# Performance work log

Measured on AMD Instinct MI355X. Metric: run time of the kernel, lower is better.

## Reference

```python
import jax, jax.numpy as jnp
import numpy as np

B, U, I, H = 4096, 6, 1024, 512
IK, IV, K = 64, 400, 4
CH, CK, CV = 4, 32, 512
NS = 4


def setup_inputs() -> dict:
    key = jax.random.key(0)
    ks = jax.random.split(key, 14)
    s = 0.02
    return dict(
        x=jax.random.normal(ks[0], (B, 1, I), jnp.float32),
        hs=jax.random.normal(ks[1], (B, U, H), jnp.float32),
        Wk=jax.random.normal(ks[2], (I, IK), jnp.float32) * s,
        bk=jnp.zeros((IK,), jnp.float32),
        Wv=jax.random.normal(ks[3], (I, IV), jnp.float32) * s,
        bv=jnp.zeros((IV,), jnp.float32),
        Wq=jax.random.normal(ks[4], (U, H, IK), jnp.float32) * s,
        Wq_=jax.random.normal(ks[5], (U, H, CH * CK), jnp.float32) * s,
        Wk_=jax.random.normal(ks[6], (U, H, CH * CK), jnp.float32) * s,
        Wv_=jax.random.normal(ks[7], (U, H, CH * CV), jnp.float32) * s,
        Wo_=jax.random.normal(ks[8], (U, CH * CV, CV), jnp.float32) * s,
        sw=jax.nn.softmax(jax.random.normal(ks[9], (U, NS), jnp.float32), axis=-1),
        gru_wx=jax.random.normal(ks[10], (NS, IV, 3 * H), jnp.float32) * s,
        gru_wh=jax.random.normal(ks[11], (NS, H, 3 * H), jnp.float32) * s,
    )


def reference(x, hs, Wk, bk, Wv, bv, Wq, Wq_, Wk_, Wv_, Wo_, sw, gru_wx, gru_wh):
    b = x.shape[0]
    # append null input along token dim -> (B, 2, I)
    x2 = jnp.concatenate([x, jnp.zeros_like(x)], axis=1)
    # input attention (num_input_heads = 1)
    k_l = x2 @ Wk + bk                                   # (B,2,IK)
    v_l = x2 @ Wv + bv                                   # (B,2,IV)
    q_l = jnp.einsum('buh,uhd->bud', hs, Wq)             # (B,U,IK)
    scores = jnp.einsum('bud,btd->but', q_l, k_l) / np.sqrt(IK).astype(np.float32)
    # top-k gating on the non-null score
    not_null = scores[:, :, 0]                           # (B,U)
    _, idx = jax.lax.top_k(not_null, K)
    mask = jnp.zeros((b, U), x.dtype).at[jnp.arange(b)[:, None], idx].set(1.0)
    probs = jax.nn.softmax(scores, axis=-1)              # dropout off (eval)
    inputs = jnp.einsum('but,btv->buv', probs, v_l) * mask[:, :, None]  # (B,U,IV)
    # shared-schema GroupGRU: per-unit weights = schema mixture
    Wx = jnp.einsum('us,sio->uio', sw, gru_wx)           # (U,IV,3H)
    Wh = jnp.einsum('us,sho->uho', sw, gru_wh)           # (U,H,3H)
    gx = jnp.einsum('bui,uio->buo', inputs, Wx)
    gh = jnp.einsum('buh,uho->buo', hs, Wh)
    xr, xz, xn = jnp.split(gx, 3, axis=-1)
    hr, hz, hn = jnp.split(gh, 3, axis=-1)
    r = jax.nn.sigmoid(xr + hr)
    z = jax.nn.sigmoid(xz + hz)
    n = jnp.tanh(xn + r * hn)
    hy = n + z * (hs - n)                                # (B,U,H)
    # blocked_grad is identity in forward
    h_b = hy
    # communication attention (4 heads)
    q = jnp.einsum('buh,uho->buo', h_b, Wq_).reshape(b, U, CH, CK).transpose(0, 2, 1, 3)
    kk = jnp.einsum('buh,uho->buo', h_b, Wk_).reshape(b, U, CH, CK).transpose(0, 2, 1, 3)
    v = jnp.einsum('buh,uho->buo', h_b, Wv_).reshape(b, U, CH, CV).transpose(0, 2, 1, 3)
    att = jnp.einsum('bhqd,bhkd->bhqk', q, kk) / np.sqrt(CK).astype(np.float32)
    ap = jax.nn.softmax(att, axis=-1) * mask[:, None, :, None]  # mask query units
    ctx = jnp.einsum('bhqk,bhkd->bhqd', ap, v)           # (B,CH,U,CV)
    ctx = ctx.transpose(0, 2, 1, 3).reshape(b, U, CH * CV)
    ctx = jnp.einsum('buh,uho->buo', ctx, Wo_) + h_b     # (B,U,H)
    m = mask[:, :, None]
    hs_new = m * ctx + (1.0 - m) * hs
    return hs_new
```

## Files before the change

### kernel.cpp

```cpp
#include <hip/hip_runtime.h>
#include <cstddef>
#include <cstdint>


typedef unsigned short u16;
typedef __bf16 bf16x8 __attribute__((ext_vector_type(8)));
typedef float f32x4 __attribute__((ext_vector_type(4)));
typedef u16 u16x4 __attribute__((ext_vector_type(4)));

#define DEVFN static __device__ __forceinline__

DEVFN float ldin(const void* p, size_t i, int f) {
  return f ? (float)reinterpret_cast<const __bf16*>(p)[i]
           : reinterpret_cast<const float*>(p)[i];
}
DEVFN float bf2f(const u16* p, size_t i) {
  return (float)reinterpret_cast<const __bf16*>(p)[i];
}
DEVFN void f2bf(u16* p, size_t i, float v) {
  reinterpret_cast<__bf16*>(p)[i] = (__bf16)v;
}
DEVFN u16 bfbits(float v) {
  __bf16 b = (__bf16)v;
  return *reinterpret_cast<u16*>(&b);
}
DEVFN void gload16(const __bf16* g, __bf16* l) {
  __builtin_amdgcn_global_load_lds(
      (const __attribute__((address_space(1))) void*)g,
      (__attribute__((address_space(3))) void*)l, 16, 0, 0);
}

constexpr size_t OFF_FLAG = 0;
constexpr size_t OFF_MASK = 256;
constexpr size_t OFF_WVT  = 98560;
constexpr size_t OFF_WQKV = 1147136;
constexpr size_t OFF_WOT  = 15302912;
constexpr size_t OFF_WXCT = 27885824;
constexpr size_t OFF_WHCT = 35553536;
constexpr size_t OFF_HY   = 44990720;
constexpr size_t OFF_XB   = 70156544;
constexpr size_t OFF_HSB  = 78545152;
constexpr size_t ARENA    = 103710976;
constexpr size_t A_INP    = ARENA;
constexpr size_t A_PK     = ARENA;
constexpr size_t A_PQ     = ARENA + 4194304;
constexpr size_t A_P1     = 124158208;
constexpr size_t A_KL     = A_P1;
constexpr size_t A_QL     = A_P1 + 1048576;
constexpr size_t A_VL     = A_P1 + 7340032;

__global__ void rim_detect(const void* sw, int* flagp) {
  if (threadIdx.x == 0) {
    float s = 0.f;
    for (int i = 0; i < 24; i++)
      s += (float)reinterpret_cast<const __bf16*>(sw)[i];
    flagp[0] = (s > 5.5f && s < 6.5f) ? 1 : 0;
  }
}

__global__ __launch_bounds__(256)
void rim_cast(const void* __restrict__ in, u16* __restrict__ out, long n8,
              const int* __restrict__ flagp)
{
  const int f = flagp[0];
  long stride = (long)gridDim.x * 256;
  for (long u = (long)blockIdx.x * 256 + threadIdx.x; u < n8; u += stride) {
    if (f) {
      reinterpret_cast<uint4*>(out)[u] = reinterpret_cast<const uint4*>(in)[u];
    } else {
      f32x4 lo = reinterpret_cast<const f32x4*>(in)[u * 2];
      f32x4 hi = reinterpret_cast<const f32x4*>(in)[u * 2 + 1];
      bf16x8 r;
#pragma unroll
      for (int q = 0; q < 4; q++) { r[q] = (__bf16)lo[q]; r[q + 4] = (__bf16)hi[q]; }
      reinterpret_cast<bf16x8*>(out)[u] = r;
    }
  }
}

__global__ __launch_bounds__(256)
void rim_sgemm32(const void* __restrict__ A_, long lda, long Az,
                 const void* __restrict__ W_, long Wz,
                 float* __restrict__ P, int KC,
                 const int* __restrict__ flagp)
{
  const int f = flagp[0];
  __shared__ float As[32 * 33];
  __shared__ float Ws[32 * 68];
  const int t = threadIdx.x;
  const int m0 = blockIdx.x * 32, kc = blockIdx.y, z = blockIdx.z;
  const int Z = gridDim.z;
  const int kb = kc * KC;
  const int tx = t & 15, ty = t >> 4;

  f32x4 acc[2];
#pragma unroll
  for (int i = 0; i < 2; i++)
#pragma unroll
    for (int j = 0; j < 4; j++) acc[i][j] = 0.f;

  for (int k0 = kb; k0 < kb + KC; k0 += 32) {
#pragma unroll
    for (int j = 0; j < 4; j++) {
      int idx = t + j * 256;
      int row = idx >> 5, kk = idx & 31;
      As[row * 33 + kk] =
          ldin(A_, (size_t)(m0 + row) * lda + (size_t)z * Az + k0 + kk, f);
    }
#pragma unroll
    for (int j = 0; j < 8; j++) {
      int idx = t + j * 256;
      int kk = idx >> 6, n = idx & 63;
      Ws[kk * 68 + n] = ldin(W_, (size_t)z * Wz + (size_t)(k0 + kk) * 64 + n, f);
    }
    __syncthreads();
#pragma unroll 8
    for (int kk = 0; kk < 32; kk++) {
      f32x4 wv = *reinterpret_cast<const f32x4*>(&Ws[kk * 68 + tx * 4]);
#pragma unroll
      for (int i = 0; i < 2; i++) {
        float a = As[(ty * 2 + i) * 33 + kk];
#pragma unroll
        for (int j = 0; j < 4; j++) acc[i][j] += a * wv[j];
      }
    }
    __syncthreads();
  }
  float* Pb = P + ((size_t)kc * Z + z) * (4096 * 64);
#pragma unroll
  for (int i = 0; i < 2; i++)
    *reinterpret_cast<f32x4*>(&Pb[(size_t)(m0 + ty * 2 + i) * 64 + tx * 4]) = acc[i];
}

__global__ void rim_sreduce(const float* __restrict__ P, int NK, int Z,
                            float* __restrict__ C, long ldc, long Cz,
                            const void* __restrict__ bias,
                            const int* __restrict__ flagp, long total)
{
  const int f = flagp[0];
  long idx = (long)blockIdx.x * 256 + threadIdx.x;
  if (idx >= total) return;
  long z = idx / (4096 * 64);
  long r = idx - z * (4096 * 64);
  long m = r >> 6;
  int n = (int)(r & 63);
  float s = bias ? ldin(bias, n, f) : 0.f;
  for (int kc = 0; kc < NK; kc++)
    s += P[((size_t)kc * Z + z) * (4096 * 64) + r];
  C[(size_t)m * ldc + (size_t)z * Cz + n] = s;
}

template<int EPI>
__global__ __launch_bounds__(256)
void rim_gemm(const u16* __restrict__ A16, long A0, long lda, long Az,
              const u16* __restrict__ B_, long Bz,
              void* __restrict__ C_, long C0, long ldc, long Cz,
              int M, int N, int K,
              const void* __restrict__ bias,
              const u16* __restrict__ hyp,
              const float* __restrict__ maskp,
              const void* __restrict__ hsp,
              const int* __restrict__ flagp)
{
  __shared__ __align__(16) __bf16 As[2][128 * 32];
  __shared__ __align__(16) __bf16 Bs[2][128 * 32];
  const int f = flagp[0];
  const int t = threadIdx.x;

  int gx = gridDim.x, gy = gridDim.y;
  int nwg = gx * gy * (int)gridDim.z;
  int wg = blockIdx.x + gx * (blockIdx.y + gy * blockIdx.z);
  {
    int q = nwg >> 3, r = nwg & 7, xc = wg & 7, ix = wg >> 3;
    wg = (xc < r ? xc * (q + 1) : r * (q + 1) + (xc - r) * q) + ix;
  }
  const int mb = wg % gx;
  const int nb = (wg / gx) % gy;
  const int z  = wg / (gx * gy);
  const int m0 = mb * 128, n0 = nb * 128;

  const __bf16* Ab = reinterpret_cast<const __bf16*>(A16) + (size_t)A0 +
                     (size_t)z * Az + (size_t)m0 * lda;
  const __bf16* Bb = reinterpret_cast<const __bf16*>(B_) + (size_t)z * Bz +
                     (size_t)n0 * (size_t)K;

  const int lane = t & 63, w = t >> 6;
  const int srow = lane >> 2;
  const int skq  = (lane & 3) * 8;
  const __bf16* aS0 = Ab + (size_t)(w * 16 + srow) * lda + skq;
  const __bf16* aS1 = Ab + (size_t)((w + 4) * 16 + srow) * lda + skq;
  const __bf16* bS0 = Bb + (size_t)(w * 16 + srow) * (size_t)K + skq;
  const __bf16* bS1 = Bb + (size_t)((w + 4) * 16 + srow) * (size_t)K + skq;

  const int wm = (w & 1) * 64, wn = (w >> 1) * 64;
  const int lr = lane & 15, lk = (lane >> 4) * 8;

  f32x4 acc[4][4];
#pragma unroll
  for (int i = 0; i < 4; i++)
#pragma unroll
    for (int j = 0; j < 4; j++)
#pragma unroll
      for (int r = 0; r < 4; r++) acc[i][j][r] = 0.f;

  auto STAGE = [&](int buf, int k0) {
    gload16(aS0 + k0, &As[buf][w * 512]);
    gload16(aS1 + k0, &As[buf][(w + 4) * 512]);
    gload16(bS0 + k0, &Bs[buf][w * 512]);
    gload16(bS1 + k0, &Bs[buf][(w + 4) * 512]);
  };

  STAGE(0, 0);
  int cur = 0;
  for (int k0 = 0; k0 < K; k0 += 32) {
    __syncthreads();
    if (k0 + 32 < K) STAGE(cur ^ 1, k0 + 32);
    bf16x8 af[4], bg[4];
#pragma unroll
    for (int i = 0; i < 4; i++)
      af[i] = *reinterpret_cast<const bf16x8*>(&As[cur][(wm + i * 16 + lr) * 32 + lk]);
#pragma unroll
    for (int j = 0; j < 4; j++)
      bg[j] = *reinterpret_cast<const bf16x8*>(&Bs[cur][(wn + j * 16 + lr) * 32 + lk]);
#pragma unroll
    for (int i = 0; i < 4; i++)
#pragma unroll
      for (int j = 0; j < 4; j++)
        acc[i][j] = __builtin_amdgcn_mfma_f32_16x16x32_bf16(af[i], bg[j], acc[i][j], 0, 0, 0);
    cur ^= 1;
  }

  const int rq = (lane >> 4) * 4;
  const int cq = lane & 15;
#pragma unroll
  for (int i = 0; i < 4; i++) {
#pragma unroll
    for (int j = 0; j < 4; j++) {
      int cg = n0 + wn + j * 16 + cq;
      if (cg >= N) continue;
#pragma unroll
      for (int r = 0; r < 4; r++) {
        int rg = m0 + wm + i * 16 + rq + r;
        if (rg >= M) continue;
        float v = acc[i][j][r];
        size_t cidx = (size_t)rg * ldc + (size_t)z * Cz + cg;
        if constexpr (EPI == 2) {
          f2bf((u16*)C_, C0 + cidx, v + ldin(bias, cg, f));
        } else if constexpr (EPI == 3) {
          f2bf((u16*)C_, C0 + cidx, v);
        } else {
          float mk = maskp[(size_t)rg * 6 + z];
          if (mk > 0.5f) {
            float o = v + bf2f(hyp, cidx);
            if (f) f2bf((u16*)C_, C0 + cidx, o);
            else   reinterpret_cast<float*>(C_)[C0 + cidx] = o;
          } else {
            if (f) reinterpret_cast<u16*>(C_)[C0 + cidx] =
                       reinterpret_cast<const u16*>(hsp)[C0 + cidx];
            else   reinterpret_cast<float*>(C_)[C0 + cidx] =
                       reinterpret_cast<const float*>(hsp)[C0 + cidx];
          }
        }
      }
    }
  }
}

__global__ __launch_bounds__(256)
void rim_transpose(const void* __restrict__ in, u16* __restrict__ out,
                   int N, int Np, int K, long in_z, long out_z,
                   const int* __restrict__ flagp)
{
  const int f = flagp[0];
  __shared__ float tile[32][33];
  int z = blockIdx.z;
  int k0 = blockIdx.x * 32, n0 = blockIdx.y * 32;
  int c = threadIdx.x & 31, r = threadIdx.x >> 5;
  for (int rr = r; rr < 32; rr += 8) {
    int k = k0 + rr, n = n0 + c;
    tile[rr][c] = (k < K && n < N)
        ? ldin(in, (size_t)z * in_z + (size_t)k * N + n, f) : 0.f;
  }
  __syncthreads();
  for (int rr = r; rr < 32; rr += 8) {
    int n = n0 + rr, k = k0 + c;
    if (n < Np && k < K)
      f2bf(out, (size_t)z * out_z + (size_t)n * K + k, tile[c][rr]);
  }
}

__global__ __launch_bounds__(256)
void rim_gruw(const void* __restrict__ sw, const void* __restrict__ gw,
              u16* __restrict__ out, int IVp, int IVs,
              const int* __restrict__ flagp)
{
  const int f = flagp[0];
  __shared__ float lds[64 * 17];
  int u = blockIdx.z;
  int i0 = blockIdx.x * 16, o0 = blockIdx.y * 64;
  int t = threadIdx.x;
  float s0 = ldin(sw, u * 4 + 0, f), s1 = ldin(sw, u * 4 + 1, f);
  float s2 = ldin(sw, u * 4 + 2, f), s3 = ldin(sw, u * 4 + 3, f);
  int oo = t & 63, iq = t >> 6;
  size_t pl = (size_t)IVs * 1536;
#pragma unroll
  for (int r = 0; r < 4; r++) {
    int ii = iq * 4 + r;
    float acc = 0.f;
    if (i0 + ii < IVs) {
      size_t base = (size_t)(i0 + ii) * 1536 + o0 + oo;
      acc = s0 * ldin(gw, base, f) + s1 * ldin(gw, pl + base, f) +
            s2 * ldin(gw, 2 * pl + base, f) + s3 * ldin(gw, 3 * pl + base, f);
    }
    lds[oo * 17 + ii] = acc;
  }
  __syncthreads();
  int ow = t >> 2, iw = (t & 3) * 4;
  u16x4 pk;
#pragma unroll
  for (int j = 0; j < 4; j++) pk[j] = bfbits(lds[ow * 17 + iw + j]);
  *reinterpret_cast<u16x4*>(out + ((size_t)u * 1536 + o0 + ow) * IVp + i0 + iw) = pk;
}

__global__ __launch_bounds__(256)
void rim_scores(const float* __restrict__ q_l, const float* __restrict__ k_l0,
                const void* __restrict__ bk, const u16* __restrict__ v_l0,
                const void* __restrict__ bv, float* __restrict__ maskf,
                u16* __restrict__ inputs, const int* __restrict__ flagp)
{
  const int f = flagp[0];
  int b = blockIdx.x;
  int t = threadIdx.x;
  int lane = t & 63;
  __shared__ float s0[6], s1[6], sm[6], sp[6];
  if (t < 64) {
    float kv = k_l0[(size_t)b * 64 + lane];
    for (int u = 0; u < 6; u++) {
      float p = q_l[((size_t)b * 6 + u) * 64 + lane] * kv;
      for (int off = 32; off; off >>= 1) p += __shfl_down(p, off);
      if (lane == 0) s0[u] = p * 0.125f;
    }
  } else if (t < 128) {
    float kv = ldin(bk, lane, f);
    for (int u = 0; u < 6; u++) {
      float p = q_l[((size_t)b * 6 + u) * 64 + lane] * kv;
      for (int off = 32; off; off >>= 1) p += __shfl_down(p, off);
      if (lane == 0) s1[u] = p * 0.125f;
    }
  }
  __syncthreads();
  if (t == 0) {
    for (int u = 0; u < 6; u++) {
      int cnt = 0;
      for (int u2 = 0; u2 < 6; u2++)
        if (s0[u2] > s0[u] || (s0[u2] == s0[u] && u2 < u)) cnt++;
      float mk = (cnt < 4) ? 1.0f : 0.0f;
      sm[u] = mk;
      maskf[(size_t)b * 6 + u] = mk;
      sp[u] = 1.0f / (1.0f + expf(s1[u] - s0[u]));
    }
  }
  __syncthreads();
  for (int idx = t; idx < 2496; idx += 256) {
    int u = idx / 416, j = idx - u * 416;
    float val = 0.f;
    if (j < 400)
      val = sm[u] * (sp[u] * bf2f(v_l0, (size_t)b * 400 + j) +
                     (1.0f - sp[u]) * ldin(bv, j, f));
    f2bf(inputs, ((size_t)b * 6 + u) * 416 + j, val);
  }
}

__global__ void rim_gru(const u16* __restrict__ Ggx, const u16* __restrict__ Ggh,
                        const void* __restrict__ hs, long R0,
                        u16* __restrict__ hy, long total,
                        const int* __restrict__ flagp)
{
  const int f = flagp[0];
  long idx = (long)blockIdx.x * 256 + threadIdx.x;
  if (idx >= total) return;
  long bu = idx >> 9;
  int h = idx & 511;
  size_t gb = (size_t)bu * 1536 + h;
  float xr = bf2f(Ggx, gb), xz = bf2f(Ggx, gb + 512), xn = bf2f(Ggx, gb + 1024);
  float hr = bf2f(Ggh, gb), hz = bf2f(Ggh, gb + 512), hn = bf2f(Ggh, gb + 1024);
  float r = 1.f / (1.f + expf(-(xr + hr)));
  float zz = 1.f / (1.f + expf(-(xz + hz)));
  float n = tanhf(xn + r * hn);
  float hv = ldin(hs, R0 + idx, f);
  f2bf(hy, idx, n + zz * (hv - n));
}

__global__ __launch_bounds__(256)
void rim_attn(const u16* __restrict__ comb, const float* __restrict__ maskp,
              u16* __restrict__ ctx)
{
  int bl = blockIdx.x;
  int t = threadIdx.x;
  const __bf16* cb = reinterpret_cast<const __bf16*>(comb) + (size_t)bl * 13824;
  __shared__ float qs[1536];
  __shared__ float aps[144];
  __shared__ __align__(16) u16 vs[12288];
  for (int idx = t; idx < 1536; idx += 256) {
    int u = idx >> 8, r = idx & 255;
    qs[idx] = (float)cb[u * 2304 + r];
  }
  for (int idx = t; idx < 1536; idx += 256) {
    int u = idx >> 8, r = idx & 255;
    *reinterpret_cast<bf16x8*>(&vs[idx * 8]) =
        *reinterpret_cast<const bf16x8*>(cb + u * 2304 + 256 + r * 8);
  }
  __syncthreads();
  if (t < 144) {
    int h = t / 36, r6 = t % 36, uq = r6 / 6, uk = r6 % 6;
    float s = 0.f;
#pragma unroll
    for (int d = 0; d < 32; d++)
      s += qs[uq * 256 + h * 32 + d] * qs[uk * 256 + 128 + h * 32 + d];
    aps[t] = s * 0.17677669529663687f;
  }
  __syncthreads();
  if (t < 24) {
    int h = t / 6, uq = t % 6;
    float* row = &aps[h * 36 + uq * 6];
    float mx = row[0];
    for (int k = 1; k < 6; k++) mx = fmaxf(mx, row[k]);
    float e[6], sum = 0.f;
    for (int k = 0; k < 6; k++) { e[k] = expf(row[k] - mx); sum += e[k]; }
    float mk = maskp[(size_t)bl * 6 + uq] / sum;
    for (int k = 0; k < 6; k++) row[k] = e[k] * mk;
  }
  __syncthreads();
  for (int idx = t; idx < 12288; idx += 256) {
    int uq = idx >> 11, g = idx & 2047, h = g >> 9;
    const float* ar = &aps[h * 36 + uq * 6];
    float acc = 0.f;
#pragma unroll
    for (int k = 0; k < 6; k++) acc += ar[k] * bf2f(vs, k * 2048 + g);
    f2bf(ctx, ((size_t)bl * 6 + uq) * 2048 + g, acc);
  }
}

extern "C" void kernel_launch(void* const* d_in, const int* in_sizes, int n_in,
                              void* d_out, int out_size, void* d_ws, size_t ws_size,
                              hipStream_t stream)
{
  (void)in_sizes; (void)n_in; (void)out_size;
  const void* x   = d_in[0];
  const void* hs  = d_in[1];
  const void* Wk  = d_in[2];
  const void* bk  = d_in[3];
  const void* Wv  = d_in[4];
  const void* bv  = d_in[5];
  const void* Wq  = d_in[6];
  const void* Wq_ = d_in[7];
  const void* Wk_ = d_in[8];
  const void* Wv_ = d_in[9];
  const void* Wo_ = d_in[10];
  const void* sw  = d_in[11];
  const void* gwx = d_in[12];
  const void* gwh = d_in[13];
  char* ws = (char*)d_ws;

  int*   flagp = (int*)(ws + OFF_FLAG);
  float* maskf = (float*)(ws + OFF_MASK);
  u16* WvT   = (u16*)(ws + OFF_WVT);
  u16* WQKV  = (u16*)(ws + OFF_WQKV);
  u16* WoT   = (u16*)(ws + OFF_WOT);
  u16* WxcT  = (u16*)(ws + OFF_WXCT);
  u16* WhcT  = (u16*)(ws + OFF_WHCT);
  u16* hy    = (u16*)(ws + OFF_HY);
  u16* xb    = (u16*)(ws + OFF_XB);
  u16* hsb   = (u16*)(ws + OFF_HSB);
  u16* inputs = (u16*)(ws + A_INP);
  float* PK   = (float*)(ws + A_PK);
  float* PQ   = (float*)(ws + A_PQ);
  float* k_l0 = (float*)(ws + A_KL);
  float* q_l  = (float*)(ws + A_QL);
  u16* v_l0   = (u16*)(ws + A_VL);

  int R2 = 256, R3 = 256;
  {
    const int cand[5] = {4096, 2048, 1024, 512, 256};
    for (int i = 0; i < 5; i++)
      if (A_P1 + (size_t)cand[i] * 36864 <= ws_size) { R2 = cand[i]; break; }
    for (int i = 0; i < 5; i++)
      if (ARENA + (size_t)cand[i] * 52224 <= ws_size) { R3 = cand[i]; break; }
  }

  rim_detect<<<dim3(1), dim3(64), 0, stream>>>(sw, flagp);

  rim_cast<<<dim3(2048), dim3(256), 0, stream>>>(x, xb, 524288L, flagp);
  rim_cast<<<dim3(2048), dim3(256), 0, stream>>>(hs, hsb, 1572864L, flagp);

  auto T = [&](const void* in, u16* outp, int N, int Np, int K, long iz, long oz,
               int Z) {
    dim3 g((K + 31) / 32, (Np + 31) / 32, Z);
    rim_transpose<<<g, dim3(256), 0, stream>>>(in, outp, N, Np, K, iz, oz, flagp);
  };
  T(Wv, WvT, 400, 512, 1024, 0, 0, 1);
  T(Wq_, WQKV, 128, 128, 512, 65536, 1179648, 6);
  T(Wk_, WQKV + 65536, 128, 128, 512, 65536, 1179648, 6);
  T(Wv_, WQKV + 131072, 2048, 2048, 512, 1048576, 1179648, 6);
  T(Wo_, WoT, 512, 512, 2048, 1048576, 1048576, 6);
  rim_gruw<<<dim3(26, 24, 6), dim3(256), 0, stream>>>(sw, gwx, WxcT, 416, 400, flagp);
  rim_gruw<<<dim3(32, 24, 6), dim3(256), 0, stream>>>(sw, gwh, WhcT, 512, 512, flagp);

  auto G = [&](int epi, const void* A, long A0, long lda, long Az,
               const u16* B, long Bz, void* C, long C0, long ldc, long Cz,
               int M, int N, int K, int Z,
               const void* bias, const u16* hyp, const float* mp, const void* hsp) {
    dim3 g((M + 127) / 128, (N + 127) / 128, Z), blk(256);
    if (epi == 2)
      rim_gemm<2><<<g, blk, 0, stream>>>((const u16*)A, A0, lda, Az, B, Bz, C, C0,
                                         ldc, Cz, M, N, K, bias, hyp, mp, hsp, flagp);
    else if (epi == 3)
      rim_gemm<3><<<g, blk, 0, stream>>>((const u16*)A, A0, lda, Az, B, Bz, C, C0,
                                         ldc, Cz, M, N, K, bias, hyp, mp, hsp, flagp);
    else
      rim_gemm<4><<<g, blk, 0, stream>>>((const u16*)A, A0, lda, Az, B, Bz, C, C0,
                                         ldc, Cz, M, N, K, bias, hyp, mp, hsp, flagp);
  };

  rim_sgemm32<<<dim3(128, 4, 1), dim3(256), 0, stream>>>(
      x, 1024, 0, Wk, 0, PK, 256, flagp);
  rim_sgemm32<<<dim3(128, 2, 6), dim3(256), 0, stream>>>(
      hs, 3072, 512, Wq, 32768, PQ, 256, flagp);
  rim_sreduce<<<dim3(1024), dim3(256), 0, stream>>>(
      PK, 4, 1, k_l0, 64, 0, bk, flagp, 4096L * 64);
  rim_sreduce<<<dim3(6144), dim3(256), 0, stream>>>(
      PQ, 2, 6, q_l, 384, 64, nullptr, flagp, 6L * 4096 * 64);
  G(2, xb, 0, 1024, 0, WvT, 0, v_l0, 0, 400, 0, 4096, 400, 1024, 1,
    bv, nullptr, nullptr, nullptr);
  rim_scores<<<dim3(4096), dim3(256), 0, stream>>>(q_l, k_l0, bk, v_l0, bv,
                                                   maskf, inputs, flagp);

  u16* Ggx = (u16*)(ws + A_P1);
  u16* Ggh = (u16*)(ws + A_P1 + (size_t)R2 * 18432);
  for (int r0 = 0; r0 < 4096; r0 += R2) {
    G(3, hsb, (long)r0 * 3072, 3072, 512, WhcT, 786432, Ggh, 0, 9216, 1536,
      R2, 1536, 512, 6, nullptr, nullptr, nullptr, nullptr);
    G(3, inputs, (long)r0 * 2496, 2496, 416, WxcT, 638976, Ggx, 0, 9216, 1536,
      R2, 1536, 416, 6, nullptr, nullptr, nullptr, nullptr);
    long total = (long)R2 * 3072;
    rim_gru<<<dim3((unsigned)(total / 256)), dim3(256), 0, stream>>>(
        Ggx, Ggh, hs, (long)r0 * 3072, hy + (size_t)r0 * 3072, total, flagp);
  }

  u16* comb  = (u16*)(ws + ARENA);
  u16* ctx_c = (u16*)(ws + ARENA + (size_t)R3 * 27648);
  for (int r0 = 0; r0 < 4096; r0 += R3) {
    G(3, hy, (long)r0 * 3072, 3072, 512, WQKV, 1179648, comb, 0, 13824, 2304,
      R3, 2304, 512, 6, nullptr, nullptr, nullptr, nullptr);
    rim_attn<<<dim3(R3), dim3(256), 0, stream>>>(comb, maskf + (size_t)r0 * 6, ctx_c);
    G(4, ctx_c, 0, 12288, 2048, WoT, 1048576, d_out, (long)r0 * 3072, 3072, 512,
      R3, 512, 2048, 6, nullptr, hy + (size_t)r0 * 3072, maskf + (size_t)r0 * 6, hs);
  }
}
```

Before: 963.2 us.

## Use 256x256 tiles with 4-stage LDS pipeline for batched GEMMs

```diff
diff --git a/kernel.cpp b/kernel.cpp
--- a/kernel.cpp
+++ b/kernel.cpp
@@ -151,19 +151,18 @@
 }
 
 template<int EPI>
-__global__ __launch_bounds__(256)
-void rim_gemm(const u16* __restrict__ A16, long A0, long lda, long Az,
-              const u16* __restrict__ B_, long Bz,
-              void* __restrict__ C_, long C0, long ldc, long Cz,
-              int M, int N, int K,
-              const void* __restrict__ bias,
-              const u16* __restrict__ hyp,
-              const float* __restrict__ maskp,
-              const void* __restrict__ hsp,
-              const int* __restrict__ flagp)
-{
-  __shared__ __align__(16) __bf16 As[2][128 * 32];
-  __shared__ __align__(16) __bf16 Bs[2][128 * 32];
+__global__ __launch_bounds__(512, 2)
+void rim_gemm2(const u16* __restrict__ A16, long A0, long lda, long Az,
+               const u16* __restrict__ B_, long Bz,
+               void* __restrict__ C_, long C0, long ldc, long Cz,
+               int M, int N, int K,
+               const u16* __restrict__ hyp,
+               const float* __restrict__ maskp,
+               const void* __restrict__ hsp,
+               const int* __restrict__ flagp)
+{
+  __shared__ __align__(16) __bf16 As[4][256 * 32];
+  __shared__ __align__(16) __bf16 Bs[4][256 * 32];
   const int f = flagp[0];
   const int t = threadIdx.x;
 
@@ -177,7 +176,7 @@
   const int mb = wg % gx;
   const int nb = (wg / gx) % gy;
   const int z  = wg / (gx * gy);
-  const int m0 = mb * 128, n0 = nb * 128;
+  const int m0 = mb * 256, n0 = nb * 256;
 
   const __bf16* Ab = reinterpret_cast<const __bf16*>(A16) + (size_t)A0 +
                      (size_t)z * Az + (size_t)m0 * lda;
@@ -187,53 +186,80 @@
   const int lane = t & 63, w = t >> 6;
   const int srow = lane >> 2;
   const int skq  = (lane & 3) * 8;
-  const __bf16* aS0 = Ab + (size_t)(w * 16 + srow) * lda + skq;
-  const __bf16* aS1 = Ab + (size_t)((w + 4) * 16 + srow) * lda + skq;
-  const __bf16* bS0 = Bb + (size_t)(w * 16 + srow) * (size_t)K + skq;
-  const __bf16* bS1 = Bb + (size_t)((w + 4) * 16 + srow) * (size_t)K + skq;
-
-  const int wm = (w & 1) * 64, wn = (w >> 1) * 64;
+  const size_t aR0 = (size_t)(w * 16 + srow) * lda + skq;
+  const size_t aR1 = (size_t)(128 + w * 16 + srow) * lda + skq;
+  const size_t bR0 = (size_t)(w * 16 + srow) * (size_t)K + skq;
+  const size_t bR1 = (size_t)(128 + w * 16 + srow) * (size_t)K + skq;
+  const int ldsOff0 = (w * 16) * 32;
+  const int ldsOff1 = (128 + w * 16) * 32;
+
+  const int wm = (w & 1) * 128, wn = (w >> 1) * 64;
   const int lr = lane & 15, lk = (lane >> 4) * 8;
 
-  f32x4 acc[4][4];
-#pragma unroll
-  for (int i = 0; i < 4; i++)
+  f32x4 acc[8][4];
+#pragma unroll
+  for (int i = 0; i < 8; i++)
 #pragma unroll
     for (int j = 0; j < 4; j++)
 #pragma unroll
       for (int r = 0; r < 4; r++) acc[i][j][r] = 0.f;
 
-  auto STAGE = [&](int buf, int k0) {
-    gload16(aS0 + k0, &As[buf][w * 512]);
-    gload16(aS1 + k0, &As[buf][(w + 4) * 512]);
-    gload16(bS0 + k0, &Bs[buf][w * 512]);
-    gload16(bS1 + k0, &Bs[buf][(w + 4) * 512]);
+  const int NT = K >> 5;
+
+  auto STAGE = [&](int slot, int kt) {
+    const __bf16* ak = Ab + kt * 32;
+    const __bf16* bk = Bb + kt * 32;
+    gload16(ak + aR0, &As[slot][ldsOff0]);
+    gload16(ak + aR1, &As[slot][ldsOff1]);
+    gload16(bk + bR0, &Bs[slot][ldsOff0]);
+    gload16(bk + bR1, &Bs[slot][ldsOff1]);
   };
 
   STAGE(0, 0);
-  int cur = 0;
-  for (int k0 = 0; k0 < K; k0 += 32) {
-    __syncthreads();
-    if (k0 + 32 < K) STAGE(cur ^ 1, k0 + 32);
-    bf16x8 af[4], bg[4];
-#pragma unroll
-    for (int i = 0; i < 4; i++)
-      af[i] = *reinterpret_cast<const bf16x8*>(&As[cur][(wm + i * 16 + lr) * 32 + lk]);
+  if (NT > 1) STAGE(1, 1);
+  if (NT > 2) STAGE(2, 2);
+  __builtin_amdgcn_sched_barrier(0);
+  if (NT > 2)      asm volatile("s_waitcnt vmcnt(8)" ::: "memory");
+  else if (NT > 1) asm volatile("s_waitcnt vmcnt(4)" ::: "memory");
+  else             asm volatile("s_waitcnt vmcnt(0)" ::: "memory");
+  __builtin_amdgcn_s_barrier();
+  __builtin_amdgcn_sched_barrier(0);
+
+  for (int tt = 0; tt < NT; ++tt) {
+    const int slot = tt & 3;
+    if (tt + 3 < NT) STAGE((tt + 3) & 3, tt + 3);
+
+    const __bf16* Asl = &As[slot][0];
+    const __bf16* Bsl = &Bs[slot][0];
+    bf16x8 af[8], bg[4];
+#pragma unroll
+    for (int i = 0; i < 8; i++)
+      af[i] = *reinterpret_cast<const bf16x8*>(&Asl[(wm + i * 16 + lr) * 32 + lk]);
 #pragma unroll
     for (int j = 0; j < 4; j++)
-      bg[j] = *reinterpret_cast<const bf16x8*>(&Bs[cur][(wn + j * 16 + lr) * 32 + lk]);
-#pragma unroll
-    for (int i = 0; i < 4; i++)
+      bg[j] = *reinterpret_cast<const bf16x8*>(&Bsl[(wn + j * 16 + lr) * 32 + lk]);
+
+    __builtin_amdgcn_s_setprio(1);
+#pragma unroll
+    for (int i = 0; i < 8; i++)
 #pragma unroll
       for (int j = 0; j < 4; j++)
         acc[i][j] = __builtin_amdgcn_mfma_f32_16x16x32_bf16(af[i], bg[j], acc[i][j], 0, 0, 0);
-    cur ^= 1;
+    __builtin_amdgcn_s_setprio(0);
+
+    __builtin_amdgcn_sched_barrier(0);
+    if (tt + 3 < NT)      asm volatile("s_waitcnt vmcnt(8)" ::: "memory");
+    else if (tt + 2 < NT) asm volatile("s_waitcnt vmcnt(4)" ::: "memory");
+    else if (tt + 1 < NT) asm volatile("s_waitcnt vmcnt(0)" ::: "memory");
+    asm volatile("s_waitcnt lgkmcnt(0)" ::: "memory");
+    __builtin_amdgcn_s_barrier();
+    __builtin_amdgcn_sched_barrier(0);
   }
 
   const int rq = (lane >> 4) * 4;
   const int cq = lane & 15;
 #pragma unroll
-  for (int i = 0; i < 4; i++) {
+  for (int i = 0; i < 8; i++) {
 #pragma unroll
     for (int j = 0; j < 4; j++) {
       int cg = n0 + wn + j * 16 + cq;
@@ -244,9 +270,7 @@
         if (rg >= M) continue;
         float v = acc[i][j][r];
         size_t cidx = (size_t)rg * ldc + (size_t)z * Cz + cg;
-        if constexpr (EPI == 2) {
-          f2bf((u16*)C_, C0 + cidx, v + ldin(bias, cg, f));
-        } else if constexpr (EPI == 3) {
+        if constexpr (EPI == 3) {
           f2bf((u16*)C_, C0 + cidx, v);
         } else {
           float mk = maskp[(size_t)rg * 6 + z];
@@ -261,6 +285,106 @@
                        reinterpret_cast<const float*>(hsp)[C0 + cidx];
           }
         }
+      }
+    }
+  }
+}
+
+template<int EPI>
+__global__ __launch_bounds__(256)
+void rim_gemm(const u16* __restrict__ A16, long A0, long lda, long Az,
+              const u16* __restrict__ B_, long Bz,
+              void* __restrict__ C_, long C0, long ldc, long Cz,
+              int M, int N, int K,
+              const void* __restrict__ bias,
+              const u16* __restrict__ hyp,
+              const float* __restrict__ maskp,
+              const void* __restrict__ hsp,
+              const int* __restrict__ flagp)
+{
+  __shared__ __align__(16) __bf16 As[2][128 * 32];
+  __shared__ __align__(16) __bf16 Bs[2][128 * 32];
+  const int f = flagp[0];
+  const int t = threadIdx.x;
+
+  int gx = gridDim.x, gy = gridDim.y;
+  int nwg = gx * gy * (int)gridDim.z;
+  int wg = blockIdx.x + gx * (blockIdx.y + gy * blockIdx.z);
+  {
+    int q = nwg >> 3, r = nwg & 7, xc = wg & 7, ix = wg >> 3;
+    wg = (xc < r ? xc * (q + 1) : r * (q + 1) + (xc - r) * q) + ix;
+  }
+  const int mb = wg % gx;
+  const int nb = (wg / gx) % gy;
+  const int z  = wg / (gx * gy);
+  const int m0 = mb * 128, n0 = nb * 128;
+
+  const __bf16* Ab = reinterpret_cast<const __bf16*>(A16) + (size_t)A0 +
+                     (size_t)z * Az + (size_t)m0 * lda;
+  const __bf16* Bb = reinterpret_cast<const __bf16*>(B_) + (size_t)z * Bz +
+                     (size_t)n0 * (size_t)K;
+
+  const int lane = t & 63, w = t >> 6;
+  const int srow = lane >> 2;
+  const int skq  = (lane & 3) * 8;
+  const __bf16* aS0 = Ab + (size_t)(w * 16 + srow) * lda + skq;
+  const __bf16* aS1 = Ab + (size_t)((w + 4) * 16 + srow) * lda + skq;
+  const __bf16* bS0 = Bb + (size_t)(w * 16 + srow) * (size_t)K + skq;
+  const __bf16* bS1 = Bb + (size_t)((w + 4) * 16 + srow) * (size_t)K + skq;
+
+  const int wm = (w & 1) * 64, wn = (w >> 1) * 64;
+  const int lr = lane & 15, lk = (lane >> 4) * 8;
+
+  f32x4 acc[4][4];
+#pragma unroll
+  for (int i = 0; i < 4; i++)
+#pragma unroll
+    for (int j = 0; j < 4; j++)
+#pragma unroll
+      for (int r = 0; r < 4; r++) acc[i][j][r] = 0.f;
+
+  auto STAGE = [&](int buf, int k0) {
+    gload16(aS0 + k0, &As[buf][w * 512]);
+    gload16(aS1 + k0, &As[buf][(w + 4) * 512]);
+    gload16(bS0 + k0, &Bs[buf][w * 512]);
+    gload16(bS1 + k0, &Bs[buf][(w + 4) * 512]);
+  };
+
+  STAGE(0, 0);
+  int cur = 0;
+  for (int k0 = 0; k0 < K; k0 += 32) {
+    __syncthreads();
+    if (k0 + 32 < K) STAGE(cur ^ 1, k0 + 32);
+    bf16x8 af[4], bg[4];
+#pragma unroll
+    for (int i = 0; i < 4; i++)
+      af[i] = *reinterpret_cast<const bf16x8*>(&As[cur][(wm + i * 16 + lr) * 32 + lk]);
+#pragma unroll
+    for (int j = 0; j < 4; j++)
+      bg[j] = *reinterpret_cast<const bf16x8*>(&Bs[cur][(wn + j * 16 + lr) * 32 + lk]);
+#pragma unroll
+    for (int i = 0; i < 4; i++)
+#pragma unroll
+      for (int j = 0; j < 4; j++)
+        acc[i][j] = __builtin_amdgcn_mfma_f32_16x16x32_bf16(af[i], bg[j], acc[i][j], 0, 0, 0);
+    cur ^= 1;
+  }
+
+  const int rq = (lane >> 4) * 4;
+  const int cq = lane & 15;
+#pragma unroll
+  for (int i = 0; i < 4; i++) {
+#pragma unroll
+    for (int j = 0; j < 4; j++) {
+      int cg = n0 + wn + j * 16 + cq;
+      if (cg >= N) continue;
+#pragma unroll
+      for (int r = 0; r < 4; r++) {
+        int rg = m0 + wm + i * 16 + rq + r;
+        if (rg >= M) continue;
+        float v = acc[i][j][r];
+        size_t cidx = (size_t)rg * ldc + (size_t)z * Cz + cg;
+        f2bf((u16*)C_, C0 + cidx, v + ldin(bias, cg, f));
       }
     }
   }
@@ -506,20 +630,17 @@
   rim_gruw<<<dim3(26, 24, 6), dim3(256), 0, stream>>>(sw, gwx, WxcT, 416, 400, flagp);
   rim_gruw<<<dim3(32, 24, 6), dim3(256), 0, stream>>>(sw, gwh, WhcT, 512, 512, flagp);
 
-  auto G = [&](int epi, const void* A, long A0, long lda, long Az,
-               const u16* B, long Bz, void* C, long C0, long ldc, long Cz,
-               int M, int N, int K, int Z,
-               const void* bias, const u16* hyp, const float* mp, const void* hsp) {
-    dim3 g((M + 127) / 128, (N + 127) / 128, Z), blk(256);
-    if (epi == 2)
-      rim_gemm<2><<<g, blk, 0, stream>>>((const u16*)A, A0, lda, Az, B, Bz, C, C0,
-                                         ldc, Cz, M, N, K, bias, hyp, mp, hsp, flagp);
-    else if (epi == 3)
-      rim_gemm<3><<<g, blk, 0, stream>>>((const u16*)A, A0, lda, Az, B, Bz, C, C0,
-                                         ldc, Cz, M, N, K, bias, hyp, mp, hsp, flagp);
+  auto G2 = [&](int epi, const void* A, long A0, long lda, long Az,
+                const u16* B, long Bz, void* C, long C0, long ldc, long Cz,
+                int M, int N, int K, int Z,
+                const u16* hyp, const float* mp, const void* hsp) {
+    dim3 g((M + 255) / 256, (N + 255) / 256, Z), blk(512);
+    if (epi == 3)
+      rim_gemm2<3><<<g, blk, 0, stream>>>((const u16*)A, A0, lda, Az, B, Bz, C, C0,
+                                          ldc, Cz, M, N, K, hyp, mp, hsp, flagp);
     else
-      rim_gemm<4><<<g, blk, 0, stream>>>((const u16*)A, A0, lda, Az, B, Bz, C, C0,
-                                         ldc, Cz, M, N, K, bias, hyp, mp, hsp, flagp);
+      rim_gemm2<4><<<g, blk, 0, stream>>>((const u16*)A, A0, lda, Az, B, Bz, C, C0,
+                                          ldc, Cz, M, N, K, hyp, mp, hsp, flagp);
   };
 
   rim_sgemm32<<<dim3(128, 4, 1), dim3(256), 0, stream>>>(
@@ -530,18 +651,22 @@
       PK, 4, 1, k_l0, 64, 0, bk, flagp, 4096L * 64);
   rim_sreduce<<<dim3(6144), dim3(256), 0, stream>>>(
       PQ, 2, 6, q_l, 384, 64, nullptr, flagp, 6L * 4096 * 64);
-  G(2, xb, 0, 1024, 0, WvT, 0, v_l0, 0, 400, 0, 4096, 400, 1024, 1,
-    bv, nullptr, nullptr, nullptr);
+  {
+    dim3 g(32, 4, 1), blk(256);
+    rim_gemm<2><<<g, blk, 0, stream>>>(xb, 0, 1024, 0, WvT, 0, v_l0, 0, 400, 0,
+                                       4096, 400, 1024, bv, nullptr, nullptr,
+                                       nullptr, flagp);
+  }
   rim_scores<<<dim3(4096), dim3(256), 0, stream>>>(q_l, k_l0, bk, v_l0, bv,
                                                    maskf, inputs, flagp);
 
   u16* Ggx = (u16*)(ws + A_P1);
   u16* Ggh = (u16*)(ws + A_P1 + (size_t)R2 * 18432);
   for (int r0 = 0; r0 < 4096; r0 += R2) {
-    G(3, hsb, (long)r0 * 3072, 3072, 512, WhcT, 786432, Ggh, 0, 9216, 1536,
-      R2, 1536, 512, 6, nullptr, nullptr, nullptr, nullptr);
-    G(3, inputs, (long)r0 * 2496, 2496, 416, WxcT, 638976, Ggx, 0, 9216, 1536,
-      R2, 1536, 416, 6, nullptr, nullptr, nullptr, nullptr);
+    G2(3, hsb, (long)r0 * 3072, 3072, 512, WhcT, 786432, Ggh, 0, 9216, 1536,
+       R2, 1536, 512, 6, nullptr, nullptr, nullptr);
+    G2(3, inputs, (long)r0 * 2496, 2496, 416, WxcT, 638976, Ggx, 0, 9216, 1536,
+       R2, 1536, 416, 6, nullptr, nullptr, nullptr);
     long total = (long)R2 * 3072;
     rim_gru<<<dim3((unsigned)(total / 256)), dim3(256), 0, stream>>>(
         Ggx, Ggh, hs, (long)r0 * 3072, hy + (size_t)r0 * 3072, total, flagp);
@@ -550,10 +675,10 @@
   u16* comb  = (u16*)(ws + ARENA);
   u16* ctx_c = (u16*)(ws + ARENA + (size_t)R3 * 27648);
   for (int r0 = 0; r0 < 4096; r0 += R3) {
-    G(3, hy, (long)r0 * 3072, 3072, 512, WQKV, 1179648, comb, 0, 13824, 2304,
-      R3, 2304, 512, 6, nullptr, nullptr, nullptr, nullptr);
+    G2(3, hy, (long)r0 * 3072, 3072, 512, WQKV, 1179648, comb, 0, 13824, 2304,
+       R3, 2304, 512, 6, nullptr, nullptr, nullptr);
     rim_attn<<<dim3(R3), dim3(256), 0, stream>>>(comb, maskf + (size_t)r0 * 6, ctx_c);
-    G(4, ctx_c, 0, 12288, 2048, WoT, 1048576, d_out, (long)r0 * 3072, 3072, 512,
-      R3, 512, 2048, 6, nullptr, hy + (size_t)r0 * 3072, maskf + (size_t)r0 * 6, hs);
-  }
-}
+    G2(4, ctx_c, 0, 12288, 2048, WoT, 1048576, d_out, (long)r0 * 3072, 3072, 512,
+       R3, 512, 2048, 6, hy + (size_t)r0 * 3072, maskf + (size_t)r0 * 6, hs);
+  }
+}
```

Result: slower. 1.183 ms (+22.9%).

## Add 256x256 8-wave MFMA GEMM with interleaved pipeline and paired GRU launches

Applied to the files above, without the earlier changes.

```diff
diff --git a/kernel.cpp b/kernel.cpp
--- a/kernel.cpp
+++ b/kernel.cpp
@@ -36,15 +36,15 @@
 constexpr size_t OFF_WQKV = 1147136;
 constexpr size_t OFF_WOT  = 15302912;
 constexpr size_t OFF_WXCT = 27885824;
-constexpr size_t OFF_WHCT = 35553536;
-constexpr size_t OFF_HY   = 44990720;
-constexpr size_t OFF_XB   = 70156544;
-constexpr size_t OFF_HSB  = 78545152;
-constexpr size_t ARENA    = 103710976;
+constexpr size_t OFF_WHCT = 36143360;
+constexpr size_t OFF_HY   = 45580544;
+constexpr size_t OFF_XB   = 70746368;
+constexpr size_t OFF_HSB  = 79134976;
+constexpr size_t ARENA    = 104300800;
 constexpr size_t A_INP    = ARENA;
 constexpr size_t A_PK     = ARENA;
 constexpr size_t A_PQ     = ARENA + 4194304;
-constexpr size_t A_P1     = 124158208;
+constexpr size_t A_P1     = 126320896;
 constexpr size_t A_KL     = A_P1;
 constexpr size_t A_QL     = A_P1 + 1048576;
 constexpr size_t A_VL     = A_P1 + 7340032;
@@ -150,6 +150,200 @@
   C[(size_t)m * ldc + (size_t)z * Cz + n] = s;
 }
 
+template<int EPI, bool PAIR>
+__global__ __launch_bounds__(512, 2)
+void rim_gemm8(const u16* __restrict__ A1_, long A01, long lda1, long Az1,
+               const u16* __restrict__ B1_, long Bz1,
+               void* __restrict__ C1_, long C01, int K1,
+               const u16* __restrict__ A2_, long A02q, long lda2, long Az2,
+               const u16* __restrict__ B2_, long Bz2,
+               void* __restrict__ C2_, long C02, int K2,
+               long ldc, long Cz, int M, int N,
+               const u16* __restrict__ hyp,
+               const float* __restrict__ maskp,
+               const void* __restrict__ hsp,
+               const int* __restrict__ flagp)
+{
+  __shared__ __align__(16) __bf16 As[2][16384];
+  __shared__ __align__(16) __bf16 Bs[2][16384];
+  const int f = flagp[0];
+  const int t = threadIdx.x;
+
+  int gx = gridDim.x, gy = gridDim.y;
+  int nwg = gx * gy * (int)gridDim.z;
+  int wg = blockIdx.x + gx * (blockIdx.y + gy * blockIdx.z);
+  {
+    int q = nwg >> 3, r = nwg & 7, xc = wg & 7, ix = wg >> 3;
+    wg = (xc < r ? xc * (q + 1) : r * (q + 1) + (xc - r) * q) + ix;
+  }
+  const int mb = wg % gx;
+  const int nb = (wg / gx) % gy;
+  const int zz = wg / (gx * gy);
+  const int m0 = mb * 256, n0 = nb * 256;
+
+  int sel = 0, z = zz;
+  if constexpr (PAIR) { sel = (zz >= 6) ? 1 : 0; z = zz - sel * 6; }
+  const long lda = sel ? lda2 : lda1;
+  const int  K   = sel ? K2 : K1;
+  const __bf16* Ab = sel
+      ? reinterpret_cast<const __bf16*>(A2_) + (size_t)A02q + (size_t)z * Az2 +
+        (size_t)m0 * lda2
+      : reinterpret_cast<const __bf16*>(A1_) + (size_t)A01 + (size_t)z * Az1 +
+        (size_t)m0 * lda1;
+  const __bf16* Bb = sel
+      ? reinterpret_cast<const __bf16*>(B2_) + (size_t)z * Bz2 + (size_t)n0 * K
+      : reinterpret_cast<const __bf16*>(B1_) + (size_t)z * Bz1 + (size_t)n0 * K;
+  void* Cp = sel ? C2_ : C1_;
+  const long C0 = sel ? C02 : C01;
+
+  const int lane = t & 63, w = t >> 6;
+  const int lsR = lane >> 3;
+  const int lsC = (lane & 7) ^ lsR;
+  const int wm = (w & 1) * 128, wn = (w >> 1) * 64;
+  const int lr = lane & 15, lk = (lane >> 4) * 8;
+  const int sw0 = lk ^ ((lane & 7) << 3);
+  const int sw1 = (32 + lk) ^ ((lane & 7) << 3);
+
+  f32x4 acc[8][4];
+#pragma unroll
+  for (int i = 0; i < 8; i++)
+#pragma unroll
+    for (int j = 0; j < 4; j++)
+#pragma unroll
+      for (int r = 0; r < 4; r++) acc[i][j][r] = 0.f;
+
+  const int NT = K >> 6;
+
+  auto ST = [&](int bn, int kt2, int part) {
+    const size_t kc = (size_t)kt2 * 64 + (size_t)lsC * 8;
+    if (part == 0) {
+      gload16(Bb + (size_t)(w * 8 + lsR) * K + kc,        &Bs[bn][w * 512]);
+      gload16(Bb + (size_t)(64 + w * 8 + lsR) * K + kc,   &Bs[bn][4096 + w * 512]);
+    } else if (part == 1) {
+      gload16(Bb + (size_t)(128 + w * 8 + lsR) * K + kc,  &Bs[bn][8192 + w * 512]);
+      gload16(Bb + (size_t)(192 + w * 8 + lsR) * K + kc,  &Bs[bn][12288 + w * 512]);
+    } else if (part == 2) {
+      gload16(Ab + (size_t)(w * 8 + lsR) * lda + kc,      &As[bn][w * 512]);
+      gload16(Ab + (size_t)(128 + w * 8 + lsR) * lda + kc, &As[bn][8192 + w * 512]);
+    } else {
+      gload16(Ab + (size_t)(64 + w * 8 + lsR) * lda + kc,  &As[bn][4096 + w * 512]);
+      gload16(Ab + (size_t)(192 + w * 8 + lsR) * lda + kc, &As[bn][12288 + w * 512]);
+    }
+  };
+
+  bf16x8 af[4][2], bg[2][2];
+
+#define RD_A(qh)                                                               \
+  _Pragma("unroll")                                                            \
+  for (int i = 0; i < 4; i++) {                                                \
+    af[i][0] = *reinterpret_cast<const bf16x8*>(                               \
+        &Asb[(wm + (qh) * 64 + i * 16 + lr) * 64 + sw0]);                      \
+    af[i][1] = *reinterpret_cast<const bf16x8*>(                               \
+        &Asb[(wm + (qh) * 64 + i * 16 + lr) * 64 + sw1]);                      \
+  }
+#define RD_B(jh)                                                               \
+  _Pragma("unroll")                                                            \
+  for (int j = 0; j < 2; j++) {                                                \
+    bg[j][0] = *reinterpret_cast<const bf16x8*>(                               \
+        &Bsb[(wn + (jh) * 32 + j * 16 + lr) * 64 + sw0]);                      \
+    bg[j][1] = *reinterpret_cast<const bf16x8*>(                               \
+        &Bsb[(wn + (jh) * 32 + j * 16 + lr) * 64 + sw1]);                      \
+  }
+#define MM(qh, jh)                                                             \
+  __builtin_amdgcn_s_setprio(1);                                               \
+  _Pragma("unroll")                                                            \
+  for (int i = 0; i < 4; i++)                                                  \
+    _Pragma("unroll")                                                          \
+    for (int j = 0; j < 2; j++)                                                \
+      _Pragma("unroll")                                                        \
+      for (int ks = 0; ks < 2; ks++)                                           \
+        acc[(qh) * 4 + i][(jh) * 2 + j] = __builtin_amdgcn_mfma_f32_16x16x32_bf16( \
+            af[i][ks], bg[j][ks], acc[(qh) * 4 + i][(jh) * 2 + j], 0, 0, 0);   \
+  __builtin_amdgcn_s_setprio(0);
+#define LG0                                                                    \
+  asm volatile("s_waitcnt lgkmcnt(0)" ::: "memory");                           \
+  __builtin_amdgcn_sched_barrier(0);
+#define SB0 __builtin_amdgcn_sched_barrier(0);
+
+  ST(0, 0, 0); SB0; ST(0, 0, 1); SB0; ST(0, 0, 2); SB0; ST(0, 0, 3); SB0;
+  asm volatile("s_waitcnt vmcnt(2)" ::: "memory");
+  __builtin_amdgcn_s_barrier();
+  SB0;
+
+  for (int kt = 0; kt < NT; ++kt) {
+    const int cur = kt & 1, nxt = cur ^ 1;
+    const bool pre = (kt + 1 < NT);
+    const __bf16* Asb = &As[cur][0];
+    const __bf16* Bsb = &Bs[cur][0];
+
+    if (pre) ST(nxt, kt + 1, 0);
+    RD_A(0); RD_B(0);
+    LG0;
+    MM(0, 0);
+    if (pre) ST(nxt, kt + 1, 1);
+    RD_B(1);
+    LG0;
+    MM(0, 1);
+    SB0;
+    if (pre) { asm volatile("s_waitcnt vmcnt(4)" ::: "memory"); }
+    else     { asm volatile("s_waitcnt vmcnt(0)" ::: "memory"); }
+    __builtin_amdgcn_s_barrier();
+    SB0;
+    if (pre) ST(nxt, kt + 1, 2);
+    RD_A(1); RD_B(0);
+    LG0;
+    MM(1, 0);
+    if (pre) ST(nxt, kt + 1, 3);
+    RD_B(1);
+    LG0;
+    MM(1, 1);
+    if (pre) {
+      SB0;
+      asm volatile("s_waitcnt vmcnt(2)" ::: "memory");
+      __builtin_amdgcn_s_barrier();
+      SB0;
+    }
+  }
+#undef RD_A
+#undef RD_B
+#undef MM
+#undef LG0
+#undef SB0
+
+  const int rq = (lane >> 4) * 4;
+  const int cq = lane & 15;
+#pragma unroll
+  for (int i = 0; i < 8; i++) {
+#pragma unroll
+    for (int j = 0; j < 4; j++) {
+      int cg = n0 + wn + j * 16 + cq;
+      if (cg >= N) continue;
+#pragma unroll
+      for (int r = 0; r < 4; r++) {
+        int rg = m0 + wm + i * 16 + rq + r;
+        if (rg >= M) continue;
+        float v = acc[i][j][r];
+        size_t cidx = (size_t)rg * ldc + (size_t)z * Cz + cg;
+        if constexpr (EPI == 3) {
+          f2bf((u16*)Cp, C0 + cidx, v);
+        } else {
+          float mk = maskp[(size_t)rg * 6 + z];
+          if (mk > 0.5f) {
+            float o = v + bf2f(hyp, cidx);
+            if (f) f2bf((u16*)Cp, C0 + cidx, o);
+            else   reinterpret_cast<float*>(Cp)[C0 + cidx] = o;
+          } else {
+            if (f) reinterpret_cast<u16*>(Cp)[C0 + cidx] =
+                       reinterpret_cast<const u16*>(hsp)[C0 + cidx];
+            else   reinterpret_cast<float*>(Cp)[C0 + cidx] =
+                       reinterpret_cast<const float*>(hsp)[C0 + cidx];
+          }
+        }
+      }
+    }
+  }
+}
+
 template<int EPI>
 __global__ __launch_bounds__(256)
 void rim_gemm(const u16* __restrict__ A16, long A0, long lda, long Az,
@@ -157,9 +351,6 @@
               void* __restrict__ C_, long C0, long ldc, long Cz,
               int M, int N, int K,
               const void* __restrict__ bias,
-              const u16* __restrict__ hyp,
-              const float* __restrict__ maskp,
-              const void* __restrict__ hsp,
               const int* __restrict__ flagp)
 {
   __shared__ __align__(16) __bf16 As[2][128 * 32];
@@ -244,23 +435,7 @@
         if (rg >= M) continue;
         float v = acc[i][j][r];
         size_t cidx = (size_t)rg * ldc + (size_t)z * Cz + cg;
-        if constexpr (EPI == 2) {
-          f2bf((u16*)C_, C0 + cidx, v + ldin(bias, cg, f));
-        } else if constexpr (EPI == 3) {
-          f2bf((u16*)C_, C0 + cidx, v);
-        } else {
-          float mk = maskp[(size_t)rg * 6 + z];
-          if (mk > 0.5f) {
-            float o = v + bf2f(hyp, cidx);
-            if (f) f2bf((u16*)C_, C0 + cidx, o);
-            else   reinterpret_cast<float*>(C_)[C0 + cidx] = o;
-          } else {
-            if (f) reinterpret_cast<u16*>(C_)[C0 + cidx] =
-                       reinterpret_cast<const u16*>(hsp)[C0 + cidx];
-            else   reinterpret_cast<float*>(C_)[C0 + cidx] =
-                       reinterpret_cast<const float*>(hsp)[C0 + cidx];
-          }
-        }
+        f2bf((u16*)C_, C0 + cidx, v + ldin(bias, cg, f));
       }
     }
   }
@@ -361,13 +536,13 @@
     }
   }
   __syncthreads();
-  for (int idx = t; idx < 2496; idx += 256) {
-    int u = idx / 416, j = idx - u * 416;
+  for (int idx = t; idx < 2688; idx += 256) {
+    int u = idx / 448, j = idx - u * 448;
     float val = 0.f;
     if (j < 400)
       val = sm[u] * (sp[u] * bf2f(v_l0, (size_t)b * 400 + j) +
                      (1.0f - sp[u]) * ldin(bv, j, f));
-    f2bf(inputs, ((size_t)b * 6 + u) * 416 + j, val);
+    f2bf(inputs, ((size_t)b * 6 + u) * 448 + j, val);
   }
 }
 
@@ -503,24 +678,8 @@
   T(Wk_, WQKV + 65536, 128, 128, 512, 65536, 1179648, 6);
   T(Wv_, WQKV + 131072, 2048, 2048, 512, 1048576, 1179648, 6);
   T(Wo_, WoT, 512, 512, 2048, 1048576, 1048576, 6);
-  rim_gruw<<<dim3(26, 24, 6), dim3(256), 0, stream>>>(sw, gwx, WxcT, 416, 400, flagp);
+  rim_gruw<<<dim3(28, 24, 6), dim3(256), 0, stream>>>(sw, gwx, WxcT, 448, 400, flagp);
   rim_gruw<<<dim3(32, 24, 6), dim3(256), 0, stream>>>(sw, gwh, WhcT, 512, 512, flagp);
-
-  auto G = [&](int epi, const void* A, long A0, long lda, long Az,
-               const u16* B, long Bz, void* C, long C0, long ldc, long Cz,
-               int M, int N, int K, int Z,
-               const void* bias, const u16* hyp, const float* mp, const void* hsp) {
-    dim3 g((M + 127) / 128, (N + 127) / 128, Z), blk(256);
-    if (epi == 2)
-      rim_gemm<2><<<g, blk, 0, stream>>>((const u16*)A, A0, lda, Az, B, Bz, C, C0,
-                                         ldc, Cz, M, N, K, bias, hyp, mp, hsp, flagp);
-    else if (epi == 3)
-      rim_gemm<3><<<g, blk, 0, stream>>>((const u16*)A, A0, lda, Az, B, Bz, C, C0,
-                                         ldc, Cz, M, N, K, bias, hyp, mp, hsp, flagp);
-    else
-      rim_gemm<4><<<g, blk, 0, stream>>>((const u16*)A, A0, lda, Az, B, Bz, C, C0,
-                                         ldc, Cz, M, N, K, bias, hyp, mp, hsp, flagp);
-  };
 
   rim_sgemm32<<<dim3(128, 4, 1), dim3(256), 0, stream>>>(
       x, 1024, 0, Wk, 0, PK, 256, flagp);
@@ -530,18 +689,22 @@
       PK, 4, 1, k_l0, 64, 0, bk, flagp, 4096L * 64);
   rim_sreduce<<<dim3(6144), dim3(256), 0, stream>>>(
       PQ, 2, 6, q_l, 384, 64, nullptr, flagp, 6L * 4096 * 64);
-  G(2, xb, 0, 1024, 0, WvT, 0, v_l0, 0, 400, 0, 4096, 400, 1024, 1,
-    bv, nullptr, nullptr, nullptr);
+  {
+    dim3 g(32, 4, 1), blk(256);
+    rim_gemm<2><<<g, blk, 0, stream>>>(xb, 0, 1024, 0, WvT, 0, v_l0, 0, 400, 0,
+                                       4096, 400, 1024, bv, flagp);
+  }
   rim_scores<<<dim3(4096), dim3(256), 0, stream>>>(q_l, k_l0, bk, v_l0, bv,
                                                    maskf, inputs, flagp);
 
   u16* Ggx = (u16*)(ws + A_P1);
   u16* Ggh = (u16*)(ws + A_P1 + (size_t)R2 * 18432);
   for (int r0 = 0; r0 < 4096; r0 += R2) {
-    G(3, hsb, (long)r0 * 3072, 3072, 512, WhcT, 786432, Ggh, 0, 9216, 1536,
-      R2, 1536, 512, 6, nullptr, nullptr, nullptr, nullptr);
-    G(3, inputs, (long)r0 * 2496, 2496, 416, WxcT, 638976, Ggx, 0, 9216, 1536,
-      R2, 1536, 416, 6, nullptr, nullptr, nullptr, nullptr);
+    dim3 g(R2 / 256, 6, 12), blk(512);
+    rim_gemm8<3, true><<<g, blk, 0, stream>>>(
+        hsb, (long)r0 * 3072, 3072, 512, WhcT, 786432, Ggh, 0, 512,
+        inputs, (long)r0 * 2688, 2688, 448, WxcT, 688128, Ggx, 0, 448,
+        9216, 1536, R2, 1536, nullptr, nullptr, nullptr, flagp);
     long total = (long)R2 * 3072;
     rim_gru<<<dim3((unsigned)(total / 256)), dim3(256), 0, stream>>>(
         Ggx, Ggh, hs, (long)r0 * 3072, hy + (size_t)r0 * 3072, total, flagp);
@@ -550,10 +713,21 @@
   u16* comb  = (u16*)(ws + ARENA);
   u16* ctx_c = (u16*)(ws + ARENA + (size_t)R3 * 27648);
   for (int r0 = 0; r0 < 4096; r0 += R3) {
-    G(3, hy, (long)r0 * 3072, 3072, 512, WQKV, 1179648, comb, 0, 13824, 2304,
-      R3, 2304, 512, 6, nullptr, nullptr, nullptr, nullptr);
+    {
+      dim3 g(R3 / 256, 9, 6), blk(512);
+      rim_gemm8<3, false><<<g, blk, 0, stream>>>(
+          hy, (long)r0 * 3072, 3072, 512, WQKV, 1179648, comb, 0, 512,
+          hy, (long)r0 * 3072, 3072, 512, WQKV, 1179648, comb, 0, 512,
+          13824, 2304, R3, 2304, nullptr, nullptr, nullptr, flagp);
+    }
     rim_attn<<<dim3(R3), dim3(256), 0, stream>>>(comb, maskf + (size_t)r0 * 6, ctx_c);
-    G(4, ctx_c, 0, 12288, 2048, WoT, 1048576, d_out, (long)r0 * 3072, 3072, 512,
-      R3, 512, 2048, 6, nullptr, hy + (size_t)r0 * 3072, maskf + (size_t)r0 * 6, hs);
-  }
-}
+    {
+      dim3 g(R3 / 256, 2, 6), blk(512);
+      rim_gemm8<4, false><<<g, blk, 0, stream>>>(
+          ctx_c, 0, 12288, 2048, WoT, 1048576, d_out, (long)r0 * 3072, 2048,
+          ctx_c, 0, 12288, 2048, WoT, 1048576, d_out, (long)r0 * 3072, 2048,
+          3072, 512, R3, 512,
+          hy + (size_t)r0 * 3072, maskf + (size_t)r0 * 6, hs, flagp);
+    }
+  }
+}
```

Result: slower. 1.157 ms (+20.2%).
